# Performance work log

Hardware: AMD Instinct MI355X
Metric: run time of the kernel (lower is better)

Reference implementation:

```python
import jax, jax.numpy as jnp
import numpy as np

N_NODES = 100000
N_EDGES = 1600000
N_GRAPHS = 1000
D_IN = 64
D_HID = 64
D_OUT = 8


def _glorot(k, shape):
    lim = float(np.sqrt(6.0 / (shape[0] + shape[1])))
    return jax.random.uniform(k, shape, jnp.float32, -lim, lim)


def setup_inputs() -> dict:
    key = jax.random.key(0)
    ks = jax.random.split(key, 12)
    x = jax.random.normal(ks[0], (N_NODES, D_IN), jnp.float32)
    edge_index = jax.random.randint(ks[1], (2, N_EDGES), 0, N_NODES, jnp.int32)
    batch = jnp.sort(jax.random.randint(ks[2], (N_NODES,), 0, N_GRAPHS, jnp.int32))
    return {
        "x": x,
        "edge_index": edge_index,
        "batch": batch,
        "W1": _glorot(ks[3], (D_IN, D_HID)),
        "b1": jnp.zeros((D_HID,), jnp.float32),
        "W2": _glorot(ks[4], (D_HID, D_HID)),
        "b2": jnp.zeros((D_HID,), jnp.float32),
        "lw1": _glorot(ks[5], (D_HID, D_HID // 2)),
        "lb1": jnp.zeros((D_HID // 2,), jnp.float32),
        "lw2": _glorot(ks[6], (D_HID // 2, D_OUT)),
        "lb2": jnp.zeros((D_OUT,), jnp.float32),
    }


def reference(x, edge_index, batch, W1, b1, W2, b2, lw1, lb1, lw2, lb2):
    # --- GCN normalization (PyG defaults: add self-loops, sym norm) ---
    loop = jnp.arange(N_NODES, dtype=edge_index.dtype)
    src = jnp.concatenate([edge_index[0], loop])
    dst = jnp.concatenate([edge_index[1], loop])
    deg = jax.ops.segment_sum(jnp.ones_like(dst, jnp.float32), dst, num_segments=N_NODES)
    dinv = jnp.where(deg > 0, jax.lax.rsqrt(jnp.maximum(deg, 1.0)), 0.0)
    norm = dinv[src] * dinv[dst]  # [E+N]

    def gcn_conv(h, W, b):
        h = h @ W  # [N, d]
        msg = h[src] * norm[:, None]  # gather along edges
        return jax.ops.segment_sum(msg, dst, num_segments=N_NODES) + b

    h = jax.nn.relu(gcn_conv(x, W1, b1))
    h = gcn_conv(h, W2, b2)

    # --- global mean pool per graph ---
    counts = jax.ops.segment_sum(jnp.ones((N_NODES,), jnp.float32), batch, num_segments=N_GRAPHS)
    pooled = jax.ops.segment_sum(h, batch, num_segments=N_GRAPHS) / jnp.maximum(counts, 1.0)[:, None]

    # --- MLP head (dropout = identity in eval) ---
    z = jax.nn.relu(pooled @ lw1 + lb1)
    return z @ lw2 + lb2
```

## Files before the change

### kernel.cpp

```cpp
#include <hip/hip_runtime.h>

static constexpr int NN  = 100000;
static constexpr int NE  = 1600000;
static constexpr int NG  = 1000;
static constexpr int D   = 64;
static constexpr int DH  = 32;
static constexpr int DO  = 8;
static constexpr int BKT = 128;
static constexpr int NBK = (NN + BKT - 1) / BKT;
static constexpr int CAP = 2560;
static constexpr int CHUNK = 4096;
static constexpr int NCH = (NE + CHUNK - 1) / CHUNK;
static constexpr int MAXW = 13504;
static constexpr int MAPS = MAXW * 8;

typedef __attribute__((ext_vector_type(8))) short bf16x8;
typedef __attribute__((ext_vector_type(4))) float f32x4;

__device__ __forceinline__ float b2f(unsigned short u) {
    return __uint_as_float(((unsigned int)u) << 16);
}
__device__ __forceinline__ unsigned short f2b(float f) {
    unsigned int u = __float_as_uint(f);
    u += 0x7FFFu + ((u >> 16) & 1u);
    return (unsigned short)(u >> 16);
}
__device__ __forceinline__ uint4 pack8(const unsigned short* h) {
    uint4 u;
    u.x = (unsigned)h[0] | ((unsigned)h[1] << 16);
    u.y = (unsigned)h[2] | ((unsigned)h[3] << 16);
    u.z = (unsigned)h[4] | ((unsigned)h[5] << 16);
    u.w = (unsigned)h[6] | ((unsigned)h[7] << 16);
    return u;
}

__global__ __launch_bounds__(1024) void
k_prepw(const float* __restrict__ W1, const float* __restrict__ W2,
        const int* __restrict__ batch,
        unsigned short* __restrict__ wtbuf, int* __restrict__ gcur,
        int* __restrict__ lbg, int* __restrict__ wbase, int* __restrict__ map) {
    __shared__ int bnd[NG + 1];
    __shared__ int tsum[256];
    int t = threadIdx.x;
    int b = blockIdx.x;
    if (b == 0) {
        for (int i = t; i < NBK; i += 1024) gcur[i] = 0;
    } else if (b == 3) {
        for (int g = t; g <= NG; g += 1024) {
            int lo = 0, hi = NN;
            while (lo < hi) { int m = (lo + hi) >> 1; if (batch[m] < g) lo = m + 1; else hi = m; }
            bnd[g] = lo;
        }
        __syncthreads();
        int s = 0, loc[4];
        if (t < 256) {
#pragma unroll
            for (int j = 0; j < 4; ++j) {
                int g = t * 4 + j;
                int pw = (g < NG) ? ((bnd[g + 1] - bnd[g] + 7) >> 3) : 0;
                loc[j] = s; s += pw;
            }
            tsum[t] = s;
        }
        __syncthreads();
        for (int o = 1; o < 256; o <<= 1) {
            int a = (t < 256 && t >= o) ? tsum[t - o] : 0;
            __syncthreads();
            if (t < 256) tsum[t] += a;
            __syncthreads();
        }
        if (t < 256) {
            int base = (t > 0) ? tsum[t - 1] : 0;
#pragma unroll
            for (int j = 0; j < 4; ++j) {
                int g = t * 4 + j;
                if (g < NG) wbase[g] = base + loc[j];
            }
            if (t == 255) wbase[NG] = tsum[255];
        }
        if (t <= NG) lbg[t] = bnd[t];
    } else if (b >= 4) {
        int4 m4 = {-1, -1, -1, -1};
        for (int i = (b - 4) * 1024 + t; i < MAPS / 4; i += 8 * 1024)
            ((int4*)map)[i] = m4;
    } else {
        if (t < 256) {
            const float* W = (b == 2) ? W2 : W1;
            unsigned short* WtHi = wtbuf + (size_t)(b - 1) * 8192;
            unsigned short* WtLo = WtHi + 4096;
            int n = t >> 2, k0 = (t & 3) * 16;
            unsigned short hi[16], lo[16];
#pragma unroll
            for (int i = 0; i < 16; ++i) {
                float v = W[(k0 + i) * 64 + n];
                hi[i] = f2b(v);
                lo[i] = f2b(v - b2f(hi[i]));
            }
            ((uint4*)WtHi)[n * 8 + (t & 3) * 2]     = pack8(hi);
            ((uint4*)WtHi)[n * 8 + (t & 3) * 2 + 1] = pack8(hi + 8);
            ((uint4*)WtLo)[n * 8 + (t & 3) * 2]     = pack8(lo);
            ((uint4*)WtLo)[n * 8 + (t & 3) * 2 + 1] = pack8(lo + 8);
        }
    }
}

__global__ __launch_bounds__(128) void
k_fillmap(const int* __restrict__ lbg, const int* __restrict__ wbase,
          int* __restrict__ map) {
    int g = blockIdx.x;
    int base = wbase[g] * 8;
    int lb = lbg[g], n = lbg[g + 1] - lb;
    int padded = (n + 7) & ~7;
    for (int i = threadIdx.x; i < padded; i += 128)
        map[base + i] = (i < n) ? (lb + i) : -1;
}

__global__ __launch_bounds__(512) void
k_bin(const int* __restrict__ src, const int* __restrict__ dst,
      int* __restrict__ gcur, int* __restrict__ ebuf) {
    __shared__ int lcnt[NBK];
    __shared__ int lbase[NBK];
    int t = threadIdx.x;
    long base = (long)blockIdx.x * CHUNK;
    for (int b = t; b < NBK; b += 512) lcnt[b] = 0;
    __syncthreads();
    int pk[8], bk[8], of[8];
#pragma unroll
    for (int j = 0; j < 8; ++j) {
        long i = base + j * 512 + t;
        if (i < NE) {
            int d = dst[i];
            bk[j] = d >> 7;
            pk[j] = src[i] * BKT + (d & (BKT - 1));
            of[j] = atomicAdd(&lcnt[bk[j]], 1);
        } else bk[j] = -1;
    }
    __syncthreads();
    for (int b = t; b < NBK; b += 512) {
        int c = lcnt[b];
        if (c) lbase[b] = b * CAP + atomicAdd(&gcur[b], c);
    }
    __syncthreads();
#pragma unroll
    for (int j = 0; j < 8; ++j)
        if (bk[j] >= 0) ebuf[lbase[bk[j]] + of[j]] = pk[j];
}

__global__ __launch_bounds__(512) void
k_csrdeg(const int* __restrict__ gcur, const int* __restrict__ ebuf,
         int* __restrict__ rowptr, int* __restrict__ deg, float* __restrict__ dinv,
         int* __restrict__ csr) {
    __shared__ int hist[BKT];
    __shared__ int sc[BKT];
    __shared__ int lcur[BKT];
    int b = blockIdx.x, t = threadIdx.x;
    if (t < BKT) hist[t] = 0;
    __syncthreads();
    int beg = b * CAP;
    int end = beg + gcur[b];
    for (int e = beg + t; e < end; e += 512)
        atomicAdd(&hist[ebuf[e] & (BKT - 1)], 1);
    __syncthreads();
    if (t < BKT) sc[t] = hist[t];
    __syncthreads();
    for (int o = 1; o < BKT; o <<= 1) {
        int a = (t < BKT && t >= o) ? sc[t - o] : 0;
        __syncthreads();
        if (t < BKT) sc[t] += a;
        __syncthreads();
    }
    int v0 = b * BKT;
    if (t < BKT) {
        int v = v0 + t;
        if (v < NN) {
            int excl = beg + sc[t] - hist[t];
            rowptr[v] = excl;
            deg[v]    = hist[t];
            dinv[v]   = rsqrtf((float)(hist[t] + 1));
            lcur[t]   = excl;
        }
    }
    __syncthreads();
    for (int e = beg + t; e < end; e += 512) {
        int p = ebuf[e];
        int slot = atomicAdd(&lcur[p & (BKT - 1)], 1);
        csr[slot] = p >> 7;
    }
}

__global__ __launch_bounds__(256) void
k_mm_mfma(const float* __restrict__ Ain, const unsigned short* __restrict__ wt,
          const float* __restrict__ dinv, uint4* __restrict__ out) {
    __shared__ unsigned short smem[4 * 64 * 72];
    unsigned short* Ahi  = smem;
    unsigned short* Alo  = smem + 4608;
    unsigned short* WtHi = smem + 9216;
    unsigned short* WtLo = smem + 13824;
    int t = threadIdx.x;
    int r = t >> 2, cc = t & 3, c0 = cc * 16;
    long n0 = (long)blockIdx.x * 64;
    {
        const uint4* H = (const uint4*)wt;
        const uint4* L = (const uint4*)(wt + 4096);
        uint4* dh = (uint4*)&WtHi[r * 72 + c0];
        uint4* dl = (uint4*)&WtLo[r * 72 + c0];
        dh[0] = H[r * 8 + cc * 2]; dh[1] = H[r * 8 + cc * 2 + 1];
        dl[0] = L[r * 8 + cc * 2]; dl[1] = L[r * 8 + cc * 2 + 1];
    }
    {
        long n = n0 + r; if (n >= NN) n = NN - 1;
        const float4* X = (const float4*)Ain;
        unsigned short hi[16], lo[16];
#pragma unroll
        for (int i = 0; i < 4; ++i) {
            float4 v = X[n * 16 + cc * 4 + i];
            float vv[4] = {v.x, v.y, v.z, v.w};
#pragma unroll
            for (int j = 0; j < 4; ++j) {
                unsigned short h = f2b(vv[j]);
                hi[i * 4 + j] = h;
                lo[i * 4 + j] = f2b(vv[j] - b2f(h));
            }
        }
        uint4* dh = (uint4*)&Ahi[r * 72 + c0];
        uint4* dl = (uint4*)&Alo[r * 72 + c0];
        dh[0] = pack8(hi); dh[1] = pack8(hi + 8);
        dl[0] = pack8(lo); dl[1] = pack8(lo + 8);
    }
    __syncthreads();
    int lane = t & 63, w = t >> 6;
    int q = lane >> 4, m = lane & 15;
    f32x4 acc[4] = {{0.f,0.f,0.f,0.f},{0.f,0.f,0.f,0.f},{0.f,0.f,0.f,0.f},{0.f,0.f,0.f,0.f}};
#pragma unroll
    for (int s = 0; s < 2; ++s) {
        int ko = s * 32 + q * 8;
        bf16x8 ah = *(const bf16x8*)&Ahi[(w * 16 + m) * 72 + ko];
        bf16x8 al = *(const bf16x8*)&Alo[(w * 16 + m) * 72 + ko];
#pragma unroll
        for (int c = 0; c < 4; ++c) {
            bf16x8 bh = *(const bf16x8*)&WtHi[(c * 16 + m) * 72 + ko];
            bf16x8 bl = *(const bf16x8*)&WtLo[(c * 16 + m) * 72 + ko];
            acc[c] = __builtin_amdgcn_mfma_f32_16x16x32_bf16(ah, bh, acc[c], 0, 0, 0);
            acc[c] = __builtin_amdgcn_mfma_f32_16x16x32_bf16(ah, bl, acc[c], 0, 0, 0);
            acc[c] = __builtin_amdgcn_mfma_f32_16x16x32_bf16(al, bh, acc[c], 0, 0, 0);
        }
    }
    __syncthreads();
    float* Ct = (float*)smem;
#pragma unroll
    for (int c = 0; c < 4; ++c)
#pragma unroll
        for (int rr = 0; rr < 4; ++rr)
            Ct[(w * 16 + q * 4 + rr) * 68 + c * 16 + m] = acc[c][rr];
    __syncthreads();
    {
        long n = n0 + r;
        if (n < NN) {
            float dv = dinv[n];
            unsigned short ob[16];
#pragma unroll
            for (int i = 0; i < 4; ++i) {
                float4 v = *(const float4*)&Ct[r * 68 + c0 + i * 4];
                ob[i * 4 + 0] = f2b(v.x * dv); ob[i * 4 + 1] = f2b(v.y * dv);
                ob[i * 4 + 2] = f2b(v.z * dv); ob[i * 4 + 3] = f2b(v.w * dv);
            }
            out[n * 8 + cc * 2]     = pack8(ob);
            out[n * 8 + cc * 2 + 1] = pack8(ob + 8);
        }
    }
}

__global__ __launch_bounds__(512) void
k_aggmm(const int* __restrict__ rowptr, const int* __restrict__ deg,
        const int* __restrict__ csr,
        const uint4* __restrict__ g4, const float* __restrict__ dinv,
        const float* __restrict__ bias, const unsigned short* __restrict__ wt,
        uint4* __restrict__ out) {
    __shared__ unsigned short smem[3 * 4608];
    unsigned short* Ahi  = smem;
    unsigned short* WtHi = smem + 4608;
    unsigned short* WtLo = smem + 9216;
    int t = threadIdx.x;
    long n0 = (long)blockIdx.x * 64;
    if (t < 256) {
        int r = t >> 2, cc = t & 3, c0 = cc * 16;
        const uint4* H = (const uint4*)wt;
        const uint4* L = (const uint4*)(wt + 4096);
        uint4* dh = (uint4*)&WtHi[r * 72 + c0];
        uint4* dl = (uint4*)&WtLo[r * 72 + c0];
        dh[0] = H[r * 8 + cc * 2]; dh[1] = H[r * 8 + cc * 2 + 1];
        dl[0] = L[r * 8 + cc * 2]; dl[1] = L[r * 8 + cc * 2 + 1];
    }
    int lane = t & 63, w = t >> 6;
    int fg = lane & 7, slot = lane >> 3;
    int ln = w * 8 + slot;
    long v = n0 + ln;
    int vc = (v < NN) ? (int)v : NN - 1;
    int beg = rowptr[vc];
    int len = (v < NN) ? deg[vc] : 0;
    int lmax = len;
    lmax = max(lmax, __shfl_xor(lmax, 8));
    lmax = max(lmax, __shfl_xor(lmax, 16));
    lmax = max(lmax, __shfl_xor(lmax, 32));
    float acc[8];
    {
        uint4 sv = g4[(long)vc * 8 + fg];
        if (v >= NN) { sv.x = sv.y = sv.z = sv.w = 0u; }
        acc[0] = __uint_as_float(sv.x << 16); acc[1] = __uint_as_float(sv.x & 0xFFFF0000u);
        acc[2] = __uint_as_float(sv.y << 16); acc[3] = __uint_as_float(sv.y & 0xFFFF0000u);
        acc[4] = __uint_as_float(sv.z << 16); acc[5] = __uint_as_float(sv.z & 0xFFFF0000u);
        acc[6] = __uint_as_float(sv.w << 16); acc[7] = __uint_as_float(sv.w & 0xFFFF0000u);
    }
    for (int e = 0; e < lmax; e += 8) {
#pragma unroll
        for (int j = 0; j < 8; ++j) {
            int ee = e + j;
            float m = (ee < len) ? 1.f : 0.f;
            int idx = beg + ((ee < len) ? ee : 0);
            int srcn = csr[idx];
            uint4 a = g4[(long)srcn * 8 + fg];
            acc[0] += m * __uint_as_float(a.x << 16);
            acc[1] += m * __uint_as_float(a.x & 0xFFFF0000u);
            acc[2] += m * __uint_as_float(a.y << 16);
            acc[3] += m * __uint_as_float(a.y & 0xFFFF0000u);
            acc[4] += m * __uint_as_float(a.z << 16);
            acc[5] += m * __uint_as_float(a.z & 0xFFFF0000u);
            acc[6] += m * __uint_as_float(a.w << 16);
            acc[7] += m * __uint_as_float(a.w & 0xFFFF0000u);
        }
    }
    {
        float dv = dinv[vc];
        unsigned short ob[8];
#pragma unroll
        for (int k = 0; k < 8; ++k) {
            float x = fmaxf(acc[k] * dv + bias[fg * 8 + k], 0.f);
            ob[k] = f2b(x);
        }
        *(uint4*)&Ahi[ln * 72 + fg * 8] = pack8(ob);
    }
    __syncthreads();
    int q = lane >> 4, m = lane & 15;
    int rs = (w & 3) * 16;
    int cb0 = (w >> 2) * 2;
    f32x4 c2[2] = {{0.f,0.f,0.f,0.f},{0.f,0.f,0.f,0.f}};
#pragma unroll
    for (int s = 0; s < 2; ++s) {
        int ko = s * 32 + q * 8;
        bf16x8 ah = *(const bf16x8*)&Ahi[(rs + m) * 72 + ko];
#pragma unroll
        for (int c = 0; c < 2; ++c) {
            bf16x8 bh = *(const bf16x8*)&WtHi[((cb0 + c) * 16 + m) * 72 + ko];
            bf16x8 bl = *(const bf16x8*)&WtLo[((cb0 + c) * 16 + m) * 72 + ko];
            c2[c] = __builtin_amdgcn_mfma_f32_16x16x32_bf16(ah, bh, c2[c], 0, 0, 0);
            c2[c] = __builtin_amdgcn_mfma_f32_16x16x32_bf16(ah, bl, c2[c], 0, 0, 0);
        }
    }
    __syncthreads();
    float* Ct = (float*)smem;
#pragma unroll
    for (int c = 0; c < 2; ++c)
#pragma unroll
        for (int rr = 0; rr < 4; ++rr)
            Ct[(rs + q * 4 + rr) * 68 + (cb0 + c) * 16 + m] = c2[c][rr];
    __syncthreads();
    {
        int r = t >> 3, c8 = (t & 7) * 8;
        long n = n0 + r;
        if (n < NN) {
            float dv = dinv[n];
            float4 a = *(const float4*)&Ct[r * 68 + c8];
            float4 b = *(const float4*)&Ct[r * 68 + c8 + 4];
            unsigned short ob[8] = {f2b(a.x * dv), f2b(a.y * dv), f2b(a.z * dv), f2b(a.w * dv),
                                    f2b(b.x * dv), f2b(b.y * dv), f2b(b.z * dv), f2b(b.w * dv)};
            out[n * 8 + (t & 7)] = pack8(ob);
        }
    }
}

__global__ __launch_bounds__(256) void
k_agg2pool(const int* __restrict__ rowptr, const int* __restrict__ deg,
           const int* __restrict__ csr,
           const uint4* __restrict__ g4, const float* __restrict__ dinv,
           const int* __restrict__ map, float* __restrict__ partial) {
    int t = threadIdx.x;
    int lane = t & 63;
    int fg = lane & 7;
    int slot = lane >> 3;
    int w = blockIdx.x * 4 + (t >> 6);
    int v = map[w * 8 + slot];
    int vc = (v < 0) ? 0 : v;
    int beg = rowptr[vc];
    int len = (v < 0) ? 0 : deg[vc];
    int lmax = len;
    lmax = max(lmax, __shfl_xor(lmax, 8));
    lmax = max(lmax, __shfl_xor(lmax, 16));
    lmax = max(lmax, __shfl_xor(lmax, 32));
    float acc[8];
    {
        uint4 sv = g4[(long)vc * 8 + fg];
        if (v < 0) { sv.x = sv.y = sv.z = sv.w = 0u; }
        acc[0] = __uint_as_float(sv.x << 16); acc[1] = __uint_as_float(sv.x & 0xFFFF0000u);
        acc[2] = __uint_as_float(sv.y << 16); acc[3] = __uint_as_float(sv.y & 0xFFFF0000u);
        acc[4] = __uint_as_float(sv.z << 16); acc[5] = __uint_as_float(sv.z & 0xFFFF0000u);
        acc[6] = __uint_as_float(sv.w << 16); acc[7] = __uint_as_float(sv.w & 0xFFFF0000u);
    }
    for (int e = 0; e < lmax; e += 8) {
#pragma unroll
        for (int j = 0; j < 8; ++j) {
            int ee = e + j;
            float m = (ee < len) ? 1.f : 0.f;
            int idx2 = beg + ((ee < len) ? ee : 0);
            int srcn = csr[idx2];
            uint4 a = g4[(long)srcn * 8 + fg];
            acc[0] += m * __uint_as_float(a.x << 16);
            acc[1] += m * __uint_as_float(a.x & 0xFFFF0000u);
            acc[2] += m * __uint_as_float(a.y << 16);
            acc[3] += m * __uint_as_float(a.y & 0xFFFF0000u);
            acc[4] += m * __uint_as_float(a.z << 16);
            acc[5] += m * __uint_as_float(a.z & 0xFFFF0000u);
            acc[6] += m * __uint_as_float(a.w << 16);
            acc[7] += m * __uint_as_float(a.w & 0xFFFF0000u);
        }
    }
    float dv = dinv[vc];
#pragma unroll
    for (int k = 0; k < 8; ++k) {
        acc[k] *= dv;
        acc[k] += __shfl_xor(acc[k], 8);
        acc[k] += __shfl_xor(acc[k], 16);
        acc[k] += __shfl_xor(acc[k], 32);
    }
    if (slot == 0) {
        float4* p4 = (float4*)&partial[(long)w * 64];
        f32x4 a = {acc[0], acc[1], acc[2], acc[3]};
        f32x4 b = {acc[4], acc[5], acc[6], acc[7]};
        p4[fg * 2]     = *(float4*)&a;
        p4[fg * 2 + 1] = *(float4*)&b;
    }
}

__global__ void k_head(const float* __restrict__ partial,
                       const int* __restrict__ lbg, const int* __restrict__ wbase,
                       const float* __restrict__ b2,
                       const float* __restrict__ lw1, const float* __restrict__ lb1,
                       const float* __restrict__ lw2, const float* __restrict__ lb2,
                       float* __restrict__ out) {
    __shared__ float pl[D];
    __shared__ float z[DH];
    int g = blockIdx.x;
    int t = threadIdx.x;
    int w0 = wbase[g], w1 = wbase[g + 1];
    int cnt = lbg[g + 1] - lbg[g];
    float s = 0.f;
    for (int w = w0; w < w1; ++w) s += partial[(long)w * 64 + t];
    pl[t] = (cnt > 0) ? (s / (float)cnt + b2[t]) : 0.f;
    __syncthreads();
    if (t < DH) {
        float a = lb1[t];
#pragma unroll
        for (int k = 0; k < D; ++k) a += pl[k] * lw1[k * DH + t];
        z[t] = fmaxf(a, 0.f);
    }
    __syncthreads();
    if (t < DO) {
        float a = lb2[t];
#pragma unroll
        for (int j = 0; j < DH; ++j) a += z[j] * lw2[j * DO + t];
        out[g * DO + t] = a;
    }
}

extern "C" void kernel_launch(void* const* d_in, const int* in_sizes, int n_in,
                              void* d_out, int out_size, void* d_ws, size_t ws_size,
                              hipStream_t stream) {
    const float* x    = (const float*)d_in[0];
    const int*   ei   = (const int*)  d_in[1];
    const int*   batch= (const int*)  d_in[2];
    const float* W1   = (const float*)d_in[3];
    const float* b1   = (const float*)d_in[4];
    const float* W2   = (const float*)d_in[5];
    const float* b2   = (const float*)d_in[6];
    const float* lw1  = (const float*)d_in[7];
    const float* lb1  = (const float*)d_in[8];
    const float* lw2  = (const float*)d_in[9];
    const float* lb2  = (const float*)d_in[10];
    float* out = (float*)d_out;

    const int* srcv = ei;
    const int* dstv = ei + NE;

    char* ws = (char*)d_ws;
    size_t off = 0;
    auto alloc = [&](size_t bytes) {
        void* p = ws + off;
        off = (off + bytes + 255) & ~(size_t)255;
        return p;
    };
    int*   gcur   = (int*)  alloc((size_t)NBK * 4);
    int*   rowptr = (int*)  alloc((size_t)NN * 4);
    int*   deg    = (int*)  alloc((size_t)NN * 4);
    int*   csr    = (int*)  alloc((size_t)NBK * CAP * 4);
    float* dinv   = (float*)alloc((size_t)NN * 4);
    int*   lbg    = (int*)  alloc((size_t)(NG + 1) * 4);
    int*   wbase  = (int*)  alloc((size_t)(NG + 1) * 4);
    int*   map    = (int*)  alloc((size_t)MAPS * 4);
    float* partial= (float*)alloc((size_t)MAXW * D * 4);
    unsigned short* wtbuf = (unsigned short*)alloc((size_t)4 * 4096 * 2);
    unsigned short* bufA = (unsigned short*)alloc((size_t)NN * D * 2);
    unsigned short* bufB = (unsigned short*)alloc((size_t)NN * D * 2);
    int*   ebuf   = (int*)bufA;

    k_prepw  <<<12, 1024, 0, stream>>>(W1, W2, batch, wtbuf, gcur, lbg, wbase, map);
    k_fillmap<<<NG, 128, 0, stream>>>(lbg, wbase, map);
    k_bin    <<<NCH, 512, 0, stream>>>(srcv, dstv, gcur, ebuf);
    k_csrdeg <<<NBK, 512, 0, stream>>>(gcur, ebuf, rowptr, deg, dinv, csr);

    const int MMB = (NN + 63) / 64;

    k_mm_mfma<<<MMB, 256, 0, stream>>>(x, wtbuf, dinv, (uint4*)bufA);
    k_aggmm<<<MMB, 512, 0, stream>>>(rowptr, deg, csr, (const uint4*)bufA, dinv, b1,
                                     wtbuf + 8192, (uint4*)bufB);
    k_agg2pool<<<MAXW / 4, 256, 0, stream>>>(rowptr, deg, csr, (const uint4*)bufB, dinv,
                                             map, partial);
    k_head<<<NG, 64, 0, stream>>>(partial, lbg, wbase, b2, lw1, lb1, lw2, lb2, out);
}
```

Measured before the change: 212.9 us.

## Sort edges by source band in CSR build and fold map fill into prep kernel

The CSR build kernel now stages each bucket's edges in shared memory and counting-sorts them by source-node band (src>>9) before scattering into CSR. Within each row, edges then come out roughly ordered by source, which should give the later gather kernels better locality on the feature table. Separately, the map-fill kernel launch is removed: block 3 of the prep kernel fills the pool map itself, using a binary search per slot. This saves one launch but serialises the whole map fill onto a single block and adds a barrier per 512-edge chunk in the scatter loop.

```diff
diff --git a/kernel.cpp b/kernel.cpp
--- a/kernel.cpp
+++ b/kernel.cpp
@@ -13,6 +13,7 @@
 static constexpr int NCH = (NE + CHUNK - 1) / CHUNK;
 static constexpr int MAXW = 13504;
 static constexpr int MAPS = MAXW * 8;
+static constexpr int NBAND = ((NN - 1) >> 9) + 1;
 
 typedef __attribute__((ext_vector_type(8))) short bf16x8;
 typedef __attribute__((ext_vector_type(4))) float f32x4;
@@ -40,6 +41,7 @@
         unsigned short* __restrict__ wtbuf, int* __restrict__ gcur,
         int* __restrict__ lbg, int* __restrict__ wbase, int* __restrict__ map) {
     __shared__ int bnd[NG + 1];
+    __shared__ int wb[NG + 1];
     __shared__ int tsum[256];
     int t = threadIdx.x;
     int b = blockIdx.x;
@@ -74,15 +76,23 @@
 #pragma unroll
             for (int j = 0; j < 4; ++j) {
                 int g = t * 4 + j;
-                if (g < NG) wbase[g] = base + loc[j];
+                if (g < NG) wb[g] = base + loc[j];
             }
-            if (t == 255) wbase[NG] = tsum[255];
-        }
-        if (t <= NG) lbg[t] = bnd[t];
-    } else if (b >= 4) {
-        int4 m4 = {-1, -1, -1, -1};
-        for (int i = (b - 4) * 1024 + t; i < MAPS / 4; i += 8 * 1024)
-            ((int4*)map)[i] = m4;
+            if (t == 255) wb[NG] = tsum[255];
+        }
+        __syncthreads();
+        for (int g = t; g <= NG; g += 1024) { wbase[g] = wb[g]; lbg[g] = bnd[g]; }
+        int tot = wb[NG] * 8;
+        for (int sI = t; sI < tot; sI += 1024) {
+            int w8 = sI >> 3;
+            int lo = 0, hi = NG - 1;
+            while (lo < hi) { int m = (lo + hi + 1) >> 1; if (wb[m] <= w8) lo = m; else hi = m - 1; }
+            int g = lo;
+            int i = sI - wb[g] * 8;
+            int n = bnd[g + 1] - bnd[g];
+            map[sI] = (i < n) ? (bnd[g] + i) : -1;
+        }
+        for (int sI = tot + t; sI < MAPS; sI += 1024) map[sI] = -1;
     } else {
         if (t < 256) {
             const float* W = (b == 2) ? W2 : W1;
@@ -104,17 +114,6 @@
     }
 }
 
-__global__ __launch_bounds__(128) void
-k_fillmap(const int* __restrict__ lbg, const int* __restrict__ wbase,
-          int* __restrict__ map) {
-    int g = blockIdx.x;
-    int base = wbase[g] * 8;
-    int lb = lbg[g], n = lbg[g + 1] - lb;
-    int padded = (n + 7) & ~7;
-    for (int i = threadIdx.x; i < padded; i += 128)
-        map[base + i] = (i < n) ? (lb + i) : -1;
-}
-
 __global__ __launch_bounds__(512) void
 k_bin(const int* __restrict__ src, const int* __restrict__ dst,
       int* __restrict__ gcur, int* __restrict__ ebuf) {
@@ -150,25 +149,38 @@
 k_csrdeg(const int* __restrict__ gcur, const int* __restrict__ ebuf,
          int* __restrict__ rowptr, int* __restrict__ deg, float* __restrict__ dinv,
          int* __restrict__ csr) {
+    __shared__ int earr[CAP];
+    __shared__ int esrt[CAP];
     __shared__ int hist[BKT];
     __shared__ int sc[BKT];
     __shared__ int lcur[BKT];
+    __shared__ int bh[NBAND];
+    __shared__ int bs[NBAND];
     int b = blockIdx.x, t = threadIdx.x;
     if (t < BKT) hist[t] = 0;
+    for (int i = t; i < NBAND; i += 512) bh[i] = 0;
     __syncthreads();
     int beg = b * CAP;
-    int end = beg + gcur[b];
-    for (int e = beg + t; e < end; e += 512)
-        atomicAdd(&hist[ebuf[e] & (BKT - 1)], 1);
+    int cnt = gcur[b];
+    for (int e = t; e < cnt; e += 512) {
+        int p = ebuf[beg + e];
+        earr[e] = p;
+        atomicAdd(&hist[p & (BKT - 1)], 1);
+        atomicAdd(&bh[p >> 16], 1);
+    }
     __syncthreads();
     if (t < BKT) sc[t] = hist[t];
-    __syncthreads();
-    for (int o = 1; o < BKT; o <<= 1) {
-        int a = (t < BKT && t >= o) ? sc[t - o] : 0;
+    if (t < NBAND) bs[t] = bh[t];
+    __syncthreads();
+    for (int o = 1; o < 256; o <<= 1) {
+        int a1 = (t < BKT && t >= o) ? sc[t - o] : 0;
+        int a2 = (t < NBAND && t >= o) ? bs[t - o] : 0;
         __syncthreads();
-        if (t < BKT) sc[t] += a;
+        if (t < BKT) sc[t] += a1;
+        if (t < NBAND) bs[t] += a2;
         __syncthreads();
     }
+    if (t < NBAND) bh[t] = bs[t] - bh[t];
     int v0 = b * BKT;
     if (t < BKT) {
         int v = v0 + t;
@@ -181,10 +193,20 @@
         }
     }
     __syncthreads();
-    for (int e = beg + t; e < end; e += 512) {
-        int p = ebuf[e];
-        int slot = atomicAdd(&lcur[p & (BKT - 1)], 1);
-        csr[slot] = p >> 7;
+    for (int e = t; e < cnt; e += 512) {
+        int p = earr[e];
+        int pos = atomicAdd(&bh[p >> 16], 1);
+        esrt[pos] = p;
+    }
+    __syncthreads();
+    for (int base2 = 0; base2 < cnt; base2 += 512) {
+        int e = base2 + t;
+        int p = (e < cnt) ? esrt[e] : -1;
+        if (p >= 0) {
+            int slot = atomicAdd(&lcur[p & (BKT - 1)], 1);
+            csr[slot] = p >> 7;
+        }
+        __syncthreads();
     }
 }
 
@@ -511,8 +533,7 @@
     unsigned short* bufB = (unsigned short*)alloc((size_t)NN * D * 2);
     int*   ebuf   = (int*)bufA;
 
-    k_prepw  <<<12, 1024, 0, stream>>>(W1, W2, batch, wtbuf, gcur, lbg, wbase, map);
-    k_fillmap<<<NG, 128, 0, stream>>>(lbg, wbase, map);
+    k_prepw  <<<4, 1024, 0, stream>>>(W1, W2, batch, wtbuf, gcur, lbg, wbase, map);
     k_bin    <<<NCH, 512, 0, stream>>>(srcv, dstv, gcur, ebuf);
     k_csrdeg <<<NBK, 512, 0, stream>>>(gcur, ebuf, rowptr, deg, dinv, csr);
 
```

Measured after the change: 289.8 us. 1.36x slower.
